# Optimization experiments

Measured on AMD Instinct MI355X. Metric: run time of the kernel, lower is better.

## Reference

```python
import jax, jax.numpy as jnp
import numpy as np

B, D, H = 32768, 256, 8
DH = D // H
SCALE = 1.0 / float(np.sqrt(DH))
# neighbor indices: for query node i, context = the other 3 nodes (in order)
NEIGH = np.array([[1, 2, 3], [0, 2, 3], [0, 1, 3], [0, 1, 2]], dtype=np.int32)


def setup_inputs() -> dict:
    key = jax.random.key(0)
    ks = jax.random.split(key, 6)
    s = 0.02
    mk = lambda k: jax.random.normal(k, (D, D), jnp.float32) * s
    return {
        "tokens": jax.random.normal(ks[0], (B, 4, D), jnp.float32),
        "Wq": mk(ks[1]),
        "Wk": mk(ks[2]),
        "Wv": mk(ks[3]),
        "Wr": mk(ks[4]),
        "Wo": mk(ks[5]),
        "ln_g": jnp.ones((D,), jnp.float32),
        "ln_b": jnp.zeros((D,), jnp.float32),
    }


def reference(tokens, Wq, Wk, Wv, Wr, Wo, ln_g, ln_b):
    # tokens: [B,4,D]. All 4 modality queries share one GCA block (share_gca=True),
    # so we batch the 4-node complete-graph message passing into one pass.
    neigh = jnp.asarray(NEIGH)
    ctx = tokens[:, neigh]                    # [B,4,3,D]
    Q = tokens @ Wq.T                         # [B,4,D]
    K = ctx @ Wk.T                            # [B,4,3,D]
    V = ctx @ Wv.T
    R = ctx @ Wr.T
    V_eff = jax.nn.sigmoid(R) * V             # gated values
    Qh = Q.reshape(B, 4, H, DH)
    Kh = K.reshape(B, 4, 3, H, DH)
    Vh = V_eff.reshape(B, 4, 3, H, DH)
    scores = jnp.einsum('bihd,bilhd->bihl', Qh, Kh) * SCALE   # [B,4,H,3]
    attn = jax.nn.softmax(scores, axis=-1)    # dropout = identity (eval mode)
    out = jnp.einsum('bihl,bilhd->bihd', attn, Vh).reshape(B, 4, D)
    out = out @ Wo.T
    y = tokens + out                          # residual
    mu = y.mean(-1, keepdims=True)
    var = y.var(-1, keepdims=True)
    y = (y - mu) / jnp.sqrt(var + 1e-5) * ln_g + ln_b   # LayerNorm
    # attn: [B,4,H,3] -> per-query attn maps (attn[:, i] == attn for modality-i query, [B,H,1,3] squeezed)
    return y, attn
```

## Files before the change

### kernel.cpp

```cpp
#include <hip/hip_runtime.h>
#include <stdint.h>


#define D_DIM   256
#define H_NUM   8
#define DH      32
#define RT      64
#define NTHR    512
#define ROWS_TOT 131072
#define Y_SZ    33554432
#define SCALE_F 0.17677669529663687f
#define W_ELEMS 65536
#define WS_NEED (5 * W_ELEMS * 2)

#define SX_LD   264
#define SQK_LD  776
#define KOFF    256
#define VOFF    512
#define SY_LD   260

typedef __attribute__((ext_vector_type(8))) short bf16x8;
typedef __attribute__((ext_vector_type(4))) float f32x4;

__device__ __forceinline__ float b2f(uint16_t s) {
    union { uint32_t u; float f; } c; c.u = ((uint32_t)s) << 16; return c.f;
}
__device__ __forceinline__ uint16_t f2b(float f) {
    union { float f; uint32_t u; } c; c.f = f;
    return (uint16_t)((c.u + 0x7fffu + ((c.u >> 16) & 1u)) >> 16);
}
__device__ __forceinline__ bf16x8 cvt8(const float* p) {
    const float4 a = *(const float4*)p;
    const float4 b = *(const float4*)(p + 4);
    bf16x8 r;
    r[0] = (short)f2b(a.x); r[1] = (short)f2b(a.y);
    r[2] = (short)f2b(a.z); r[3] = (short)f2b(a.w);
    r[4] = (short)f2b(b.x); r[5] = (short)f2b(b.y);
    r[6] = (short)f2b(b.z); r[7] = (short)f2b(b.w);
    return r;
}

__global__ __launch_bounds__(256)
void conv_weights(const float* __restrict__ Wq, const float* __restrict__ Wk,
                  const float* __restrict__ Wv, const float* __restrict__ Wr,
                  const float* __restrict__ Wo, uint16_t* __restrict__ dst)
{
    const int m = blockIdx.x >> 6;
    const float* src = (m == 0) ? Wq : (m == 1) ? Wk : (m == 2) ? Wv
                     : (m == 3) ? Wr : Wo;
    const int base = (blockIdx.x & 63) * 1024 + threadIdx.x * 4;
    const float4 v = *(const float4*)&src[base];
    uint2 pk;
    pk.x = (uint32_t)f2b(v.x) | ((uint32_t)f2b(v.y) << 16);
    pk.y = (uint32_t)f2b(v.z) | ((uint32_t)f2b(v.w) << 16);
    *(uint2*)&dst[(size_t)m * W_ELEMS + base] = pk;
}

template<bool WBF16>
__global__ __launch_bounds__(NTHR, 2)
void cmaa_fused(const float* __restrict__ tok,
                const float* __restrict__ Wq, const float* __restrict__ Wk,
                const float* __restrict__ Wv, const float* __restrict__ Wr,
                const float* __restrict__ Wo,
                const uint16_t* __restrict__ wbf,
                const float* __restrict__ lng, const float* __restrict__ lnb,
                float* __restrict__ outp)
{
    __shared__ __align__(16) uint16_t sX [RT * SX_LD];
    __shared__ __align__(16) uint16_t sQK[RT * SQK_LD];

    const int tid  = threadIdx.x;
    const int wv   = tid >> 6;
    const int lane = tid & 63;
    const int l15  = lane & 15;
    const int quad = lane >> 4;
    const int R0   = blockIdx.x * RT;

    {
        const float* g = tok + (size_t)R0 * D_DIM;
        #pragma unroll
        for (int t = tid; t < RT * (D_DIM / 8); t += NTHR) {
            const int row = t >> 5, c = t & 31;
            *(bf16x8*)&sX[row * SX_LD + c * 8] = cvt8(&g[row * D_DIM + c * 8]);
        }
    }
    __syncthreads();

    {
        const int colbase = (wv & 3) * 64;
        const float*    WF0 = (wv < 4) ? Wq : Wv;
        const float*    WF1 = (wv < 4) ? Wk : Wr;
        const uint16_t* WB0 = wbf + (size_t)((wv < 4) ? 0 : 2) * W_ELEMS;
        const uint16_t* WB1 = WB0 + W_ELEMS;

        f32x4 acc[2][4][4];
        #pragma unroll
        for (int m = 0; m < 2; ++m)
            #pragma unroll
            for (int mt = 0; mt < 4; ++mt)
                #pragma unroll
                for (int nt = 0; nt < 4; ++nt)
                    acc[m][mt][nt] = (f32x4){0.f, 0.f, 0.f, 0.f};

        #pragma unroll
        for (int kk = 0; kk < 8; ++kk) {
            const int k0 = kk * 32;
            bf16x8 a[4];
            #pragma unroll
            for (int mt = 0; mt < 4; ++mt)
                a[mt] = *(const bf16x8*)&sX[(mt * 16 + l15) * SX_LD + k0 + quad * 8];

            bf16x8 bw[4];
            #pragma unroll
            for (int nt = 0; nt < 4; ++nt) {
                const int wrow = colbase + nt * 16 + l15;
                if constexpr (WBF16)
                    bw[nt] = *(const bf16x8*)&WB0[(size_t)wrow * D_DIM + k0 + quad * 8];
                else
                    bw[nt] = cvt8(&WF0[(size_t)wrow * D_DIM + k0 + quad * 8]);
            }
            #pragma unroll
            for (int nt = 0; nt < 4; ++nt)
                #pragma unroll
                for (int mt = 0; mt < 4; ++mt)
                    acc[0][mt][nt] = __builtin_amdgcn_mfma_f32_16x16x32_bf16(a[mt], bw[nt], acc[0][mt][nt], 0, 0, 0);

            #pragma unroll
            for (int nt = 0; nt < 4; ++nt) {
                const int wrow = colbase + nt * 16 + l15;
                if constexpr (WBF16)
                    bw[nt] = *(const bf16x8*)&WB1[(size_t)wrow * D_DIM + k0 + quad * 8];
                else
                    bw[nt] = cvt8(&WF1[(size_t)wrow * D_DIM + k0 + quad * 8]);
            }
            #pragma unroll
            for (int nt = 0; nt < 4; ++nt)
                #pragma unroll
                for (int mt = 0; mt < 4; ++mt)
                    acc[1][mt][nt] = __builtin_amdgcn_mfma_f32_16x16x32_bf16(a[mt], bw[nt], acc[1][mt][nt], 0, 0, 0);
        }

        if (wv < 4) {
            #pragma unroll
            for (int mt = 0; mt < 4; ++mt)
                #pragma unroll
                for (int nt = 0; nt < 4; ++nt)
                    #pragma unroll
                    for (int r = 0; r < 4; ++r) {
                        const int row = mt * 16 + quad * 4 + r;
                        const int col = colbase + nt * 16 + l15;
                        sQK[row * SQK_LD + col]        = f2b(acc[0][mt][nt][r]);
                        sQK[row * SQK_LD + KOFF + col] = f2b(acc[1][mt][nt][r]);
                    }
        } else {
            #pragma unroll
            for (int mt = 0; mt < 4; ++mt)
                #pragma unroll
                for (int nt = 0; nt < 4; ++nt)
                    #pragma unroll
                    for (int r = 0; r < 4; ++r) {
                        const int row = mt * 16 + quad * 4 + r;
                        const int col = colbase + nt * 16 + l15;
                        const float vv = acc[0][mt][nt][r];
                        const float rr = acc[1][mt][nt][r];
                        const float sig = 1.f / (1.f + __expf(-rr));
                        sQK[row * SQK_LD + VOFF + col] = f2b(vv * sig);
                    }
        }
    }
    __syncthreads();

    {
        const int r  = tid >> 3;
        const int h  = tid & 7;
        const int gr = R0 + r;
        const int i  = r & 3;
        const int rb = r & ~3;
        int rn[3];
        #pragma unroll
        for (int l = 0; l < 3; ++l) { const int jj = l + (l >= i); rn[l] = rb + jj; }

        float q[DH];
        #pragma unroll
        for (int t = 0; t < 4; ++t) {
            const bf16x8 v = *(const bf16x8*)&sQK[r * SQK_LD + h * DH + t * 8];
            #pragma unroll
            for (int j = 0; j < 8; ++j) q[t * 8 + j] = b2f((uint16_t)v[j]);
        }

        float sc[3];
        #pragma unroll
        for (int l = 0; l < 3; ++l) {
            float s = 0.f;
            #pragma unroll
            for (int t = 0; t < 4; ++t) {
                const bf16x8 v = *(const bf16x8*)&sQK[rn[l] * SQK_LD + KOFF + h * DH + t * 8];
                #pragma unroll
                for (int j = 0; j < 8; ++j) s += q[t * 8 + j] * b2f((uint16_t)v[j]);
            }
            sc[l] = s * SCALE_F;
        }
        const float mx = fmaxf(sc[0], fmaxf(sc[1], sc[2]));
        const float e0 = __expf(sc[0] - mx), e1 = __expf(sc[1] - mx), e2 = __expf(sc[2] - mx);
        const float inv = 1.f / (e0 + e1 + e2);
        const float al[3] = { e0 * inv, e1 * inv, e2 * inv };

        float* ap = outp + Y_SZ + ((size_t)gr * H_NUM + h) * 3;
        ap[0] = al[0]; ap[1] = al[1]; ap[2] = al[2];

        __syncthreads();

        #pragma unroll
        for (int t = 0; t < 4; ++t) {
            float o[8] = {0.f,0.f,0.f,0.f,0.f,0.f,0.f,0.f};
            #pragma unroll
            for (int l = 0; l < 3; ++l) {
                const bf16x8 vv = *(const bf16x8*)&sQK[rn[l] * SQK_LD + VOFF + h * DH + t * 8];
                #pragma unroll
                for (int j = 0; j < 8; ++j) o[j] += al[l] * b2f((uint16_t)vv[j]);
            }
            bf16x8 pk;
            #pragma unroll
            for (int j = 0; j < 8; ++j) pk[j] = (short)f2b(o[j]);
            *(bf16x8*)&sQK[r * SQK_LD + h * DH + t * 8] = pk;
        }
    }
    __syncthreads();

    {
        f32x4 acc3[4][2];
        #pragma unroll
        for (int mt = 0; mt < 4; ++mt)
            #pragma unroll
            for (int nt = 0; nt < 2; ++nt)
                acc3[mt][nt] = (f32x4){0.f, 0.f, 0.f, 0.f};

        const uint16_t* WoB = wbf + (size_t)4 * W_ELEMS;
        #pragma unroll
        for (int kk = 0; kk < 8; ++kk) {
            const int k0 = kk * 32;
            bf16x8 a[4];
            #pragma unroll
            for (int mt = 0; mt < 4; ++mt)
                a[mt] = *(const bf16x8*)&sQK[(mt * 16 + l15) * SQK_LD + k0 + quad * 8];
            bf16x8 bw[2];
            #pragma unroll
            for (int nt = 0; nt < 2; ++nt) {
                const int wrow = wv * 32 + nt * 16 + l15;
                if constexpr (WBF16)
                    bw[nt] = *(const bf16x8*)&WoB[(size_t)wrow * D_DIM + k0 + quad * 8];
                else
                    bw[nt] = cvt8(&Wo[(size_t)wrow * D_DIM + k0 + quad * 8]);
            }
            #pragma unroll
            for (int nt = 0; nt < 2; ++nt)
                #pragma unroll
                for (int mt = 0; mt < 4; ++mt)
                    acc3[mt][nt] = __builtin_amdgcn_mfma_f32_16x16x32_bf16(a[mt], bw[nt], acc3[mt][nt], 0, 0, 0);
        }
        __syncthreads();

        float* sY = (float*)sQK;
        #pragma unroll
        for (int mt = 0; mt < 4; ++mt)
            #pragma unroll
            for (int nt = 0; nt < 2; ++nt)
                #pragma unroll
                for (int r = 0; r < 4; ++r) {
                    const int row = mt * 16 + quad * 4 + r;
                    const int col = wv * 32 + nt * 16 + l15;
                    sY[row * SY_LD + col] = acc3[mt][nt][r] + b2f(sX[row * SX_LD + col]);
                }
    }
    __syncthreads();

    {
        const float* sY = (const float*)sQK;
        const int row = tid >> 3;
        const int sub = tid & 7;
        float vals[32];
        float s = 0.f;
        #pragma unroll
        for (int j = 0; j < 8; ++j) {
            const float4 v = *(const float4*)&sY[row * SY_LD + j * 32 + sub * 4];
            vals[j*4+0] = v.x; vals[j*4+1] = v.y; vals[j*4+2] = v.z; vals[j*4+3] = v.w;
            s += v.x + v.y + v.z + v.w;
        }
        s += __shfl_xor(s, 1); s += __shfl_xor(s, 2); s += __shfl_xor(s, 4);
        const float mean = s * (1.f / 256.f);
        float s2 = 0.f;
        #pragma unroll
        for (int j = 0; j < 32; ++j) { const float d = vals[j] - mean; s2 += d * d; }
        s2 += __shfl_xor(s2, 1); s2 += __shfl_xor(s2, 2); s2 += __shfl_xor(s2, 4);
        const float var  = fmaxf(s2 * (1.f / 256.f), 0.f);
        const float rstd = rsqrtf(var + 1e-5f);

        float* orow = outp + (size_t)(R0 + row) * D_DIM;
        #pragma unroll
        for (int j = 0; j < 8; ++j) {
            const int col = j * 32 + sub * 4;
            const float4 g4 = *(const float4*)&lng[col];
            const float4 b4 = *(const float4*)&lnb[col];
            float4 o4;
            o4.x = (vals[j*4+0] - mean) * rstd * g4.x + b4.x;
            o4.y = (vals[j*4+1] - mean) * rstd * g4.y + b4.y;
            o4.z = (vals[j*4+2] - mean) * rstd * g4.z + b4.z;
            o4.w = (vals[j*4+3] - mean) * rstd * g4.w + b4.w;
            *(float4*)&orow[col] = o4;
        }
    }
}

extern "C" void kernel_launch(void* const* d_in, const int* in_sizes, int n_in,
                              void* d_out, int out_size, void* d_ws, size_t ws_size,
                              hipStream_t stream) {
    (void)in_sizes; (void)n_in; (void)out_size;
    const float* tok = (const float*)d_in[0];
    const float* Wq  = (const float*)d_in[1];
    const float* Wk  = (const float*)d_in[2];
    const float* Wv  = (const float*)d_in[3];
    const float* Wr  = (const float*)d_in[4];
    const float* Wo  = (const float*)d_in[5];
    const float* lng = (const float*)d_in[6];
    const float* lnb = (const float*)d_in[7];
    float* outp = (float*)d_out;
    uint16_t* wbf = (uint16_t*)d_ws;

    dim3 grid(ROWS_TOT / RT), block(NTHR);
    if (ws_size >= (size_t)WS_NEED) {
        conv_weights<<<dim3(320), dim3(256), 0, stream>>>(Wq, Wk, Wv, Wr, Wo, wbf);
        cmaa_fused<true><<<grid, block, 0, stream>>>(
            tok, Wq, Wk, Wv, Wr, Wo, wbf, lng, lnb, outp);
    } else {
        cmaa_fused<false><<<grid, block, 0, stream>>>(
            tok, Wq, Wk, Wv, Wr, Wo, wbf, lng, lnb, outp);
    }
}
```

Baseline: 440.7 us.

## Double block threads and re-partition projection, attention and Wo work

Raises the block to 1024 threads so each wave computes half as many output columns in the QKVR and Wo GEMMs. Attention now uses two threads per (row, head), each covering half of the head dimension, and combines their partial dot products with a shuffle. The redundant barrier inside attention is dropped, and Wo fragments are preloaded into registers before attention so their global latency is hidden behind it. The goal is more waves in flight to hide latency, since LDS use already limits residency to one block per CU. The risk is that the tighter launch bound caps VGPRs and may cause register spills.

Result: no change. 432.8 us (-1.8%).

```diff
diff --git a/kernel.cpp b/kernel.cpp
--- a/kernel.cpp
+++ b/kernel.cpp
@@ -6,7 +6,7 @@
 #define H_NUM   8
 #define DH      32
 #define RT      64
-#define NTHR    512
+#define NTHR    1024
 #define ROWS_TOT 131072
 #define Y_SZ    33554432
 #define SCALE_F 0.17677669529663687f
@@ -57,7 +57,7 @@
 }
 
 template<bool WBF16>
-__global__ __launch_bounds__(NTHR, 2)
+__global__ __launch_bounds__(NTHR, 4)
 void cmaa_fused(const float* __restrict__ tok,
                 const float* __restrict__ Wq, const float* __restrict__ Wk,
                 const float* __restrict__ Wv, const float* __restrict__ Wr,
@@ -87,19 +87,20 @@
     __syncthreads();
 
     {
-        const int colbase = (wv & 3) * 64;
-        const float*    WF0 = (wv < 4) ? Wq : Wv;
-        const float*    WF1 = (wv < 4) ? Wk : Wr;
-        const uint16_t* WB0 = wbf + (size_t)((wv < 4) ? 0 : 2) * W_ELEMS;
+        const int  colbase = (wv & 7) * 32;
+        const bool qk = (wv < 8);
+        const float*    WF0 = qk ? Wq : Wv;
+        const float*    WF1 = qk ? Wk : Wr;
+        const uint16_t* WB0 = wbf + (size_t)(qk ? 0 : 2) * W_ELEMS;
         const uint16_t* WB1 = WB0 + W_ELEMS;
 
-        f32x4 acc[2][4][4];
+        f32x4 acc[2][4][2];
         #pragma unroll
         for (int m = 0; m < 2; ++m)
             #pragma unroll
             for (int mt = 0; mt < 4; ++mt)
                 #pragma unroll
-                for (int nt = 0; nt < 4; ++nt)
+                for (int nt = 0; nt < 2; ++nt)
                     acc[m][mt][nt] = (f32x4){0.f, 0.f, 0.f, 0.f};
 
         #pragma unroll
@@ -110,41 +111,35 @@
             for (int mt = 0; mt < 4; ++mt)
                 a[mt] = *(const bf16x8*)&sX[(mt * 16 + l15) * SX_LD + k0 + quad * 8];
 
-            bf16x8 bw[4];
-            #pragma unroll
-            for (int nt = 0; nt < 4; ++nt) {
+            bf16x8 b0[2], b1[2];
+            #pragma unroll
+            for (int nt = 0; nt < 2; ++nt) {
                 const int wrow = colbase + nt * 16 + l15;
-                if constexpr (WBF16)
-                    bw[nt] = *(const bf16x8*)&WB0[(size_t)wrow * D_DIM + k0 + quad * 8];
-                else
-                    bw[nt] = cvt8(&WF0[(size_t)wrow * D_DIM + k0 + quad * 8]);
+                if constexpr (WBF16) {
+                    b0[nt] = *(const bf16x8*)&WB0[(size_t)wrow * D_DIM + k0 + quad * 8];
+                    b1[nt] = *(const bf16x8*)&WB1[(size_t)wrow * D_DIM + k0 + quad * 8];
+                } else {
+                    b0[nt] = cvt8(&WF0[(size_t)wrow * D_DIM + k0 + quad * 8]);
+                    b1[nt] = cvt8(&WF1[(size_t)wrow * D_DIM + k0 + quad * 8]);
+                }
             }
             #pragma unroll
-            for (int nt = 0; nt < 4; ++nt)
+            for (int nt = 0; nt < 2; ++nt)
                 #pragma unroll
                 for (int mt = 0; mt < 4; ++mt)
-                    acc[0][mt][nt] = __builtin_amdgcn_mfma_f32_16x16x32_bf16(a[mt], bw[nt], acc[0][mt][nt], 0, 0, 0);
-
-            #pragma unroll
-            for (int nt = 0; nt < 4; ++nt) {
-                const int wrow = colbase + nt * 16 + l15;
-                if constexpr (WBF16)
-                    bw[nt] = *(const bf16x8*)&WB1[(size_t)wrow * D_DIM + k0 + quad * 8];
-                else
-                    bw[nt] = cvt8(&WF1[(size_t)wrow * D_DIM + k0 + quad * 8]);
-            }
-            #pragma unroll
-            for (int nt = 0; nt < 4; ++nt)
+                    acc[0][mt][nt] = __builtin_amdgcn_mfma_f32_16x16x32_bf16(a[mt], b0[nt], acc[0][mt][nt], 0, 0, 0);
+            #pragma unroll
+            for (int nt = 0; nt < 2; ++nt)
                 #pragma unroll
                 for (int mt = 0; mt < 4; ++mt)
-                    acc[1][mt][nt] = __builtin_amdgcn_mfma_f32_16x16x32_bf16(a[mt], bw[nt], acc[1][mt][nt], 0, 0, 0);
-        }
-
-        if (wv < 4) {
-            #pragma unroll
-            for (int mt = 0; mt < 4; ++mt)
-                #pragma unroll
-                for (int nt = 0; nt < 4; ++nt)
+                    acc[1][mt][nt] = __builtin_amdgcn_mfma_f32_16x16x32_bf16(a[mt], b1[nt], acc[1][mt][nt], 0, 0, 0);
+        }
+
+        if (qk) {
+            #pragma unroll
+            for (int mt = 0; mt < 4; ++mt)
+                #pragma unroll
+                for (int nt = 0; nt < 2; ++nt)
                     #pragma unroll
                     for (int r = 0; r < 4; ++r) {
                         const int row = mt * 16 + quad * 4 + r;
@@ -156,34 +151,49 @@
             #pragma unroll
             for (int mt = 0; mt < 4; ++mt)
                 #pragma unroll
-                for (int nt = 0; nt < 4; ++nt)
+                for (int nt = 0; nt < 2; ++nt)
                     #pragma unroll
                     for (int r = 0; r < 4; ++r) {
                         const int row = mt * 16 + quad * 4 + r;
                         const int col = colbase + nt * 16 + l15;
-                        const float vv = acc[0][mt][nt][r];
-                        const float rr = acc[1][mt][nt][r];
+                        const float vvv = acc[0][mt][nt][r];
+                        const float rr  = acc[1][mt][nt][r];
                         const float sig = 1.f / (1.f + __expf(-rr));
-                        sQK[row * SQK_LD + VOFF + col] = f2b(vv * sig);
+                        sQK[row * SQK_LD + VOFF + col] = f2b(vvv * sig);
                     }
         }
     }
     __syncthreads();
 
-    {
-        const int r  = tid >> 3;
-        const int h  = tid & 7;
+    bf16x8 bw3[8];
+    {
+        const uint16_t* WoB = wbf + (size_t)4 * W_ELEMS;
+        const int worow = wv * 16 + l15;
+        #pragma unroll
+        for (int kk = 0; kk < 8; ++kk) {
+            if constexpr (WBF16)
+                bw3[kk] = *(const bf16x8*)&WoB[(size_t)worow * D_DIM + kk * 32 + quad * 8];
+            else
+                bw3[kk] = cvt8(&Wo[(size_t)worow * D_DIM + kk * 32 + quad * 8]);
+        }
+    }
+
+    {
+        const int r    = tid >> 4;
+        const int h    = (tid >> 1) & 7;
+        const int half = tid & 1;
         const int gr = R0 + r;
         const int i  = r & 3;
         const int rb = r & ~3;
         int rn[3];
         #pragma unroll
         for (int l = 0; l < 3; ++l) { const int jj = l + (l >= i); rn[l] = rb + jj; }
-
-        float q[DH];
-        #pragma unroll
-        for (int t = 0; t < 4; ++t) {
-            const bf16x8 v = *(const bf16x8*)&sQK[r * SQK_LD + h * DH + t * 8];
+        const int qoff = h * DH + half * 16;
+
+        float q[16];
+        #pragma unroll
+        for (int t = 0; t < 2; ++t) {
+            const bf16x8 v = *(const bf16x8*)&sQK[r * SQK_LD + qoff + t * 8];
             #pragma unroll
             for (int j = 0; j < 8; ++j) q[t * 8 + j] = b2f((uint16_t)v[j]);
         }
@@ -193,11 +203,12 @@
         for (int l = 0; l < 3; ++l) {
             float s = 0.f;
             #pragma unroll
-            for (int t = 0; t < 4; ++t) {
-                const bf16x8 v = *(const bf16x8*)&sQK[rn[l] * SQK_LD + KOFF + h * DH + t * 8];
+            for (int t = 0; t < 2; ++t) {
+                const bf16x8 v = *(const bf16x8*)&sQK[rn[l] * SQK_LD + KOFF + qoff + t * 8];
                 #pragma unroll
                 for (int j = 0; j < 8; ++j) s += q[t * 8 + j] * b2f((uint16_t)v[j]);
             }
+            s += __shfl_xor(s, 1);
             sc[l] = s * SCALE_F;
         }
         const float mx = fmaxf(sc[0], fmaxf(sc[1], sc[2]));
@@ -205,37 +216,33 @@
         const float inv = 1.f / (e0 + e1 + e2);
         const float al[3] = { e0 * inv, e1 * inv, e2 * inv };
 
-        float* ap = outp + Y_SZ + ((size_t)gr * H_NUM + h) * 3;
-        ap[0] = al[0]; ap[1] = al[1]; ap[2] = al[2];
-
-        __syncthreads();
-
-        #pragma unroll
-        for (int t = 0; t < 4; ++t) {
+        if (half == 0) {
+            float* ap = outp + Y_SZ + ((size_t)gr * H_NUM + h) * 3;
+            ap[0] = al[0]; ap[1] = al[1]; ap[2] = al[2];
+        }
+
+        #pragma unroll
+        for (int t = 0; t < 2; ++t) {
             float o[8] = {0.f,0.f,0.f,0.f,0.f,0.f,0.f,0.f};
             #pragma unroll
             for (int l = 0; l < 3; ++l) {
-                const bf16x8 vv = *(const bf16x8*)&sQK[rn[l] * SQK_LD + VOFF + h * DH + t * 8];
+                const bf16x8 vv = *(const bf16x8*)&sQK[rn[l] * SQK_LD + VOFF + qoff + t * 8];
                 #pragma unroll
                 for (int j = 0; j < 8; ++j) o[j] += al[l] * b2f((uint16_t)vv[j]);
             }
             bf16x8 pk;
             #pragma unroll
             for (int j = 0; j < 8; ++j) pk[j] = (short)f2b(o[j]);
-            *(bf16x8*)&sQK[r * SQK_LD + h * DH + t * 8] = pk;
+            *(bf16x8*)&sQK[r * SQK_LD + qoff + t * 8] = pk;
         }
     }
     __syncthreads();
 
     {
-        f32x4 acc3[4][2];
-        #pragma unroll
-        for (int mt = 0; mt < 4; ++mt)
-            #pragma unroll
-            for (int nt = 0; nt < 2; ++nt)
-                acc3[mt][nt] = (f32x4){0.f, 0.f, 0.f, 0.f};
-
-        const uint16_t* WoB = wbf + (size_t)4 * W_ELEMS;
+        f32x4 acc3[4];
+        #pragma unroll
+        for (int mt = 0; mt < 4; ++mt) acc3[mt] = (f32x4){0.f, 0.f, 0.f, 0.f};
+
         #pragma unroll
         for (int kk = 0; kk < 8; ++kk) {
             const int k0 = kk * 32;
@@ -243,62 +250,51 @@
             #pragma unroll
             for (int mt = 0; mt < 4; ++mt)
                 a[mt] = *(const bf16x8*)&sQK[(mt * 16 + l15) * SQK_LD + k0 + quad * 8];
-            bf16x8 bw[2];
-            #pragma unroll
-            for (int nt = 0; nt < 2; ++nt) {
-                const int wrow = wv * 32 + nt * 16 + l15;
-                if constexpr (WBF16)
-                    bw[nt] = *(const bf16x8*)&WoB[(size_t)wrow * D_DIM + k0 + quad * 8];
-                else
-                    bw[nt] = cvt8(&Wo[(size_t)wrow * D_DIM + k0 + quad * 8]);
+            #pragma unroll
+            for (int mt = 0; mt < 4; ++mt)
+                acc3[mt] = __builtin_amdgcn_mfma_f32_16x16x32_bf16(a[mt], bw3[kk], acc3[mt], 0, 0, 0);
+        }
+        __syncthreads();
+
+        float* sY = (float*)sQK;
+        #pragma unroll
+        for (int mt = 0; mt < 4; ++mt)
+            #pragma unroll
+            for (int r = 0; r < 4; ++r) {
+                const int row = mt * 16 + quad * 4 + r;
+                const int col = wv * 16 + l15;
+                sY[row * SY_LD + col] = acc3[mt][r] + b2f(sX[row * SX_LD + col]);
             }
-            #pragma unroll
-            for (int nt = 0; nt < 2; ++nt)
-                #pragma unroll
-                for (int mt = 0; mt < 4; ++mt)
-                    acc3[mt][nt] = __builtin_amdgcn_mfma_f32_16x16x32_bf16(a[mt], bw[nt], acc3[mt][nt], 0, 0, 0);
-        }
-        __syncthreads();
-
-        float* sY = (float*)sQK;
-        #pragma unroll
-        for (int mt = 0; mt < 4; ++mt)
-            #pragma unroll
-            for (int nt = 0; nt < 2; ++nt)
-                #pragma unroll
-                for (int r = 0; r < 4; ++r) {
-                    const int row = mt * 16 + quad * 4 + r;
-                    const int col = wv * 32 + nt * 16 + l15;
-                    sY[row * SY_LD + col] = acc3[mt][nt][r] + b2f(sX[row * SX_LD + col]);
-                }
     }
     __syncthreads();
 
     {
         const float* sY = (const float*)sQK;
-        const int row = tid >> 3;
-        const int sub = tid & 7;
-        float vals[32];
+        const int row = tid >> 4;
+        const int sub = tid & 15;
+        float vals[16];
         float s = 0.f;
         #pragma unroll
-        for (int j = 0; j < 8; ++j) {
-            const float4 v = *(const float4*)&sY[row * SY_LD + j * 32 + sub * 4];
+        for (int j = 0; j < 4; ++j) {
+            const float4 v = *(const float4*)&sY[row * SY_LD + j * 64 + sub * 4];
             vals[j*4+0] = v.x; vals[j*4+1] = v.y; vals[j*4+2] = v.z; vals[j*4+3] = v.w;
             s += v.x + v.y + v.z + v.w;
         }
-        s += __shfl_xor(s, 1); s += __shfl_xor(s, 2); s += __shfl_xor(s, 4);
+        s += __shfl_xor(s, 1); s += __shfl_xor(s, 2);
+        s += __shfl_xor(s, 4); s += __shfl_xor(s, 8);
         const float mean = s * (1.f / 256.f);
         float s2 = 0.f;
         #pragma unroll
-        for (int j = 0; j < 32; ++j) { const float d = vals[j] - mean; s2 += d * d; }
-        s2 += __shfl_xor(s2, 1); s2 += __shfl_xor(s2, 2); s2 += __shfl_xor(s2, 4);
+        for (int j = 0; j < 16; ++j) { const float d = vals[j] - mean; s2 += d * d; }
+        s2 += __shfl_xor(s2, 1); s2 += __shfl_xor(s2, 2);
+        s2 += __shfl_xor(s2, 4); s2 += __shfl_xor(s2, 8);
         const float var  = fmaxf(s2 * (1.f / 256.f), 0.f);
         const float rstd = rsqrtf(var + 1e-5f);
 
         float* orow = outp + (size_t)(R0 + row) * D_DIM;
         #pragma unroll
-        for (int j = 0; j < 8; ++j) {
-            const int col = j * 32 + sub * 4;
+        for (int j = 0; j < 4; ++j) {
+            const int col = j * 64 + sub * 4;
             const float4 g4 = *(const float4*)&lng[col];
             const float4 b4 = *(const float4*)&lnb[col];
             float4 o4;
```
